# Kernel optimization log

Measured on AMD Instinct MI355X. Metric: run time of the kernel, lower is better.

## Reference

```python
import jax, jax.numpy as jnp
import numpy as np

TEMPERATURE = 0.1


def setup_inputs() -> dict:
    key = jax.random.key(0)
    k1, k2, k3 = jax.random.split(key, 3)
    B, C, D = 8192, 1000, 128
    features = jax.random.normal(k1, (B, D), dtype=jnp.float32)
    features = features / jnp.linalg.norm(features, axis=-1, keepdims=True)
    centers1 = jax.random.normal(k2, (C, D), dtype=jnp.float32)
    centers1 = centers1 / jnp.linalg.norm(centers1, axis=-1, keepdims=True)
    targets = jax.random.randint(k3, (B,), 0, C, dtype=jnp.int64)
    return {"centers1": centers1, "features": features, "targets": targets}


def reference(centers1, features, targets):
    B = features.shape[0]
    C = centers1.shape[0]
    dt = features.dtype

    # concatenated targets: batch targets followed by one target per class center
    t_all = jnp.concatenate([targets, jnp.arange(C, dtype=targets.dtype)])  # [B+C]
    # per-class counts over the concatenated targets (each class >= 1 from its center)
    cls_count = jnp.zeros((C,), dt).at[t_all].add(1.0)

    # positive mask [B, B+C]; zero out self-comparisons on the leading diagonal
    mask = (targets[:, None] == t_all[None, :]).astype(dt)
    logits_mask = jnp.ones((B, B + C), dt).at[jnp.arange(B), jnp.arange(B)].set(0.0)
    mask = mask * logits_mask

    feats_all = jnp.concatenate([features, centers1], axis=0)  # [B+C, D]
    logits = jnp.matmul(features, feats_all.T) / TEMPERATURE    # [B, B+C]
    logits = logits - jax.lax.stop_gradient(jnp.max(logits, axis=1, keepdims=True))

    exp_logits = jnp.exp(logits) * logits_mask
    per_ins_weight = cls_count[t_all][None, :] - mask           # [B, B+C]
    exp_logits_sum = jnp.sum(exp_logits / per_ins_weight, axis=1, keepdims=True)

    log_prob = logits - jnp.log(exp_logits_sum)
    mean_log_prob_pos = jnp.sum(mask * log_prob, axis=1) / jnp.sum(mask, axis=1)
    return -jnp.mean(mean_log_prob_pos)
```

## Files before the change

kernel.cpp:

```cpp
#include <hip/hip_runtime.h>
#include <math.h>

typedef __attribute__((ext_vector_type(8))) short short8;
typedef __attribute__((ext_vector_type(4))) float f32x4;

#define BB 8192
#define CC 1000
#define NN 9192
#define NPAD 9216
#define DD 128
#define RBW 32
#define NSPLIT 8
#define CPB 1152
#define NT 36
#define K2F 14.426950408889634f

#define WS_CLS   0
#define WS_META  1024
#define WS_SPART 37888
#define WS_PPART 103424
#define WS_F2    168960
#define WS_BS    463872

static __device__ __forceinline__ unsigned short f2bf(float x) {
    unsigned int b = __float_as_uint(x);
    unsigned int r = (b + 0x7FFFu + ((b >> 16) & 1u)) >> 16;
    return (unsigned short)r;
}
static __device__ __forceinline__ float fexp2(float x) {
    float r; asm("v_exp_f32 %0, %1" : "=v"(r) : "v"(x)); return r;
}
static __device__ __forceinline__ float flog2(float x) {
    float r; asm("v_log_f32 %0, %1" : "=v"(r) : "v"(x)); return r;
}

__global__ __launch_bounds__(1024) void prep_kernel(
    const float* __restrict__ feats, const float* __restrict__ ctrs,
    const int* __restrict__ tgt, unsigned short* __restrict__ F2,
    int* __restrict__ cls, float4* __restrict__ meta)
{
    const int tid = threadIdx.x;
    if (blockIdx.x < 144) {
        int u = blockIdx.x * 1024 + tid;
        int j = u >> 4, quad = u & 15;
        int k0 = quad * 8;
        float4 v0 = {0.f,0.f,0.f,0.f}, v1 = {0.f,0.f,0.f,0.f};
        if (j < BB) {
            v0 = *(const float4*)&feats[(size_t)j * DD + k0];
            v1 = *(const float4*)&feats[(size_t)j * DD + k0 + 4];
        } else if (j < NN) {
            v0 = *(const float4*)&ctrs[(size_t)(j - BB) * DD + k0];
            v1 = *(const float4*)&ctrs[(size_t)(j - BB) * DD + k0 + 4];
        }
        short8 o;
        o[0]=f2bf(v0.x); o[1]=f2bf(v0.y); o[2]=f2bf(v0.z); o[3]=f2bf(v0.w);
        o[4]=f2bf(v1.x); o[5]=f2bf(v1.y); o[6]=f2bf(v1.z); o[7]=f2bf(v1.w);
        size_t offb = (size_t)((((j >> 4) * 4 + (quad >> 2)) * 64 + (quad & 3) * 16 + (j & 15)) * 8);
        *(short8*)&F2[offb] = o;
        return;
    }

    __shared__ int h[1024];
    h[tid] = 0;
    __syncthreads();
    for (int i = tid; i < BB; i += 1024) atomicAdd(&h[tgt[i]], 1);
    __syncthreads();

    cls[tid] = h[tid];

    for (int j = tid; j < NPAD; j += 1024) {
        float4 m = {__int_as_float(-2), 0.f, 0.f, 0.f};
        if (j < NN) {
            int c = (j < BB) ? tgt[j] : (j - BB);
            int n = h[c] + 1;
            m.x = __int_as_float(c);
            m.y = 1.0f / (float)n;
            m.z = (n > 1) ? 1.0f / (float)(n - 1) : 0.0f;
        }
        meta[j] = m;
    }
}

static __device__ __forceinline__ void loadB32(const unsigned short* __restrict__ F2,
                                               int j0, int lane8, short8 (&buf)[8]) {
#pragma unroll
    for (int fn = 0; fn < 2; ++fn)
#pragma unroll
        for (int ks = 0; ks < 4; ++ks)
            buf[fn * 4 + ks] = *(const short8*)&F2[(size_t)(((((j0 >> 4) + fn) * 4 + ks) * 512) + lane8)];
}

static __device__ __forceinline__ void mfma32(const short8 (&af)[4][2], const short8 (&b)[8],
                                              f32x4 (&acc)[2][2]) {
    const f32x4 z4 = {0.f, 0.f, 0.f, 0.f};
#pragma unroll
    for (int fm = 0; fm < 2; ++fm)
#pragma unroll
        for (int fn = 0; fn < 2; ++fn)
            acc[fm][fn] = __builtin_amdgcn_mfma_f32_16x16x32_bf16(af[0][fm], b[fn * 4], z4, 0, 0, 0);
#pragma unroll
    for (int ks = 1; ks < 4; ++ks)
#pragma unroll
        for (int fm = 0; fm < 2; ++fm)
#pragma unroll
            for (int fn = 0; fn < 2; ++fn)
                acc[fm][fn] = __builtin_amdgcn_mfma_f32_16x16x32_bf16(
                    af[ks][fm], b[fn * 4 + ks], acc[fm][fn], 0, 0, 0);
}

template<bool DIAG>
static __device__ __forceinline__ void epi32(const f32x4 (&acc)[2][2], const float4 (&mt)[2],
                                             int j0, int l15, int rowbase,
                                             const int (&ti)[8],
                                             float (&Sl)[8], float (&Pl)[8]) {
#pragma unroll
    for (int fn = 0; fn < 2; ++fn) {
        const int tj = __float_as_int(mt[fn].x);
        const float r0 = mt[fn].y, r1 = mt[fn].z;
        const int col = j0 + fn * 16 + l15;
#pragma unroll
        for (int fm = 0; fm < 2; ++fm)
#pragma unroll
            for (int q = 0; q < 4; ++q) {
                const int x = fm * 4 + q;
                float d = acc[fm][fn][q];
                float l2 = fmaf(d, K2F, -K2F);
                float e = fexp2(l2);
                bool m = (tj == ti[x]);
                if (DIAG) {
                    bool self = (col == rowbase + fm * 16 + q);
                    if (self) { e = 0.f; m = false; }
                }
                float rw = m ? r1 : r0;
                Sl[x] = fmaf(e, rw, Sl[x]);
                Pl[x] += m ? d : 0.f;
            }
    }
}

__global__ __launch_bounds__(256, 2) void main_kernel(
    const unsigned short* __restrict__ F2, const float4* __restrict__ meta,
    float* __restrict__ S_part, float* __restrict__ P_part)
{
    const int tid  = threadIdx.x;
    const int lane = tid & 63;
    const int wave = tid >> 6;
    const int l15 = lane & 15, l4 = lane >> 4;
    const int lane8 = lane * 8;
    const int row0 = blockIdx.x * (4 * RBW) + wave * RBW;
    const int split = blockIdx.y;
    const int cb = split * CPB;
    const int rowbase = row0 + l4 * 4;

    short8 af[4][2];
#pragma unroll
    for (int fm = 0; fm < 2; ++fm)
#pragma unroll
        for (int ks = 0; ks < 4; ++ks)
            af[ks][fm] = *(const short8*)&F2[(size_t)((((row0 >> 4) + fm) * 4 + ks) * 512 + lane8)];

    int ti[8];
#pragma unroll
    for (int fm = 0; fm < 2; ++fm)
#pragma unroll
        for (int q = 0; q < 4; ++q)
            ti[fm * 4 + q] = __float_as_int(meta[rowbase + fm * 16 + q].x);

    float Sl[8], Pl[8];
#pragma unroll
    for (int x = 0; x < 8; ++x) { Sl[x] = 0.f; Pl[x] = 0.f; }

    short8 bA[8], bB[8];
    float4 mA[2], mB[2];
    loadB32(F2, cb, lane8, bA);
    mA[0] = meta[cb + l15]; mA[1] = meta[cb + 16 + l15];

#pragma unroll 1
    for (int tt = 0; tt < NT; tt += 2) {
        {
            if (tt + 1 < NT) {
                int j = cb + (tt + 1) * 32;
                loadB32(F2, j, lane8, bB);
                mB[0] = meta[j + l15]; mB[1] = meta[j + 16 + l15];
            }
            const int j0 = cb + tt * 32;
            f32x4 acc[2][2];
            mfma32(af, bA, acc);
            if (j0 == row0) epi32<true >(acc, mA, j0, l15, rowbase, ti, Sl, Pl);
            else            epi32<false>(acc, mA, j0, l15, rowbase, ti, Sl, Pl);
        }
        {
            if (tt + 2 < NT) {
                int j = cb + (tt + 2) * 32;
                loadB32(F2, j, lane8, bA);
                mA[0] = meta[j + l15]; mA[1] = meta[j + 16 + l15];
            }
            const int j0 = cb + (tt + 1) * 32;
            f32x4 acc[2][2];
            mfma32(af, bB, acc);
            if (j0 == row0) epi32<true >(acc, mB, j0, l15, rowbase, ti, Sl, Pl);
            else            epi32<false>(acc, mB, j0, l15, rowbase, ti, Sl, Pl);
        }
    }

#pragma unroll
    for (int idx = 0; idx < 8; ++idx) {
        float S = Sl[idx], P = Pl[idx];
#pragma unroll
        for (int off = 1; off < 16; off <<= 1) {
            S += __shfl_xor(S, off, 64);
            P += __shfl_xor(P, off, 64);
        }
        if (l15 == 0) {
            int row = row0 + (idx >> 2) * 16 + l4 * 4 + (idx & 3);
            S_part[(size_t)row * NSPLIT + split] = S;
            P_part[(size_t)row * NSPLIT + split] = P;
        }
    }
}

__global__ __launch_bounds__(256) void final1_kernel(
    const int* __restrict__ tgt, const int* __restrict__ cls,
    const float* __restrict__ S_part, const float* __restrict__ P_part,
    float* __restrict__ bs)
{
    const int tid = threadIdx.x;
    const int i = blockIdx.x * 256 + tid;
    float S = 0.f, P = 0.f;
    const float4* sp = (const float4*)&S_part[(size_t)i * NSPLIT];
    const float4* pp = (const float4*)&P_part[(size_t)i * NSPLIT];
#pragma unroll
    for (int q = 0; q < NSPLIT / 4; ++q) {
        float4 a = sp[q]; S += (a.x + a.y) + (a.z + a.w);
        float4 b = pp[q]; P += (b.x + b.y) + (b.z + b.w);
    }
    const float npos = (float)cls[tgt[i]];
    float lp = fmaf(K2F, P / npos, -K2F) - flog2(S);

#pragma unroll
    for (int off = 1; off < 64; off <<= 1) lp += __shfl_xor(lp, off, 64);
    __shared__ float wsum[4];
    if ((tid & 63) == 0) wsum[tid >> 6] = lp;
    __syncthreads();
    if (tid == 0) bs[blockIdx.x] = wsum[0] + wsum[1] + wsum[2] + wsum[3];
}

__global__ void final2_kernel(const float* __restrict__ bs, float* __restrict__ out) {
    const int t = threadIdx.x;
    float v = (t < 32) ? bs[t] : 0.f;
#pragma unroll
    for (int off = 1; off < 64; off <<= 1) v += __shfl_xor(v, off, 64);
    if (t == 0) out[0] = -0.6931471805599453f * (v / (float)BB);
}

extern "C" void kernel_launch(void* const* d_in, const int* in_sizes, int n_in,
                              void* d_out, int out_size, void* d_ws, size_t ws_size,
                              hipStream_t stream) {
    const float* ctrs  = (const float*)d_in[0];
    const float* feats = (const float*)d_in[1];
    const int*   tgt   = (const int*)d_in[2];
    float* out = (float*)d_out;
    float* ws  = (float*)d_ws;

    int*    cls  = (int*)(ws + WS_CLS);
    float4* meta = (float4*)(ws + WS_META);
    float*  Sp   = ws + WS_SPART;
    float*  Pp   = ws + WS_PPART;
    float*  bs   = ws + WS_BS;
    unsigned short* F2 = (unsigned short*)(ws + WS_F2);

    prep_kernel<<<dim3(145), dim3(1024), 0, stream>>>(feats, ctrs, tgt, F2, cls, meta);
    main_kernel<<<dim3(BB / (4 * RBW), NSPLIT), dim3(256), 0, stream>>>(F2, meta, Sp, Pp);
    final1_kernel<<<dim3(BB / 256), dim3(256), 0, stream>>>(tgt, cls, Sp, Pp, bs);
    final2_kernel<<<dim3(1), dim3(64), 0, stream>>>(bs, out);
}
```

Baseline: 45.43 us.

## Split positive-pair handling into sparse correction kernel, simplify dense epilogue

```diff
diff --git a/kernel.cpp b/kernel.cpp
--- a/kernel.cpp
+++ b/kernel.cpp
@@ -15,12 +15,15 @@
 #define NT 36
 #define K2F 14.426950408889634f
 
-#define WS_CLS   0
-#define WS_META  1024
-#define WS_SPART 37888
-#define WS_PPART 103424
-#define WS_F2    168960
-#define WS_BS    463872
+#define WS_CLS    0
+#define WS_OFF    1024
+#define WS_LIST   2048
+#define WS_RCP0   11264
+#define WS_SCORR  20480
+#define WS_PCORR  28672
+#define WS_SPART  36864
+#define WS_BS     102400
+#define WS_F2     102464
 
 static __device__ __forceinline__ unsigned short f2bf(float x) {
     unsigned int b = __float_as_uint(x);
@@ -37,7 +40,8 @@
 __global__ __launch_bounds__(1024) void prep_kernel(
     const float* __restrict__ feats, const float* __restrict__ ctrs,
     const int* __restrict__ tgt, unsigned short* __restrict__ F2,
-    int* __restrict__ cls, float4* __restrict__ meta)
+    int* __restrict__ cls, int* __restrict__ off, int* __restrict__ list,
+    float* __restrict__ rcp0)
 {
     const int tid = threadIdx.x;
     if (blockIdx.x < 144) {
@@ -61,23 +65,54 @@
     }
 
     __shared__ int h[1024];
+    __shared__ int s[1024];
+    __shared__ int cur[1024];
+    __shared__ int llds[NPAD];
+
     h[tid] = 0;
     __syncthreads();
     for (int i = tid; i < BB; i += 1024) atomicAdd(&h[tgt[i]], 1);
     __syncthreads();
 
-    cls[tid] = h[tid];
+    const int cnt_b = h[tid];
+    cls[tid] = cnt_b;
 
     for (int j = tid; j < NPAD; j += 1024) {
-        float4 m = {__int_as_float(-2), 0.f, 0.f, 0.f};
+        float v = 0.f;
         if (j < NN) {
             int c = (j < BB) ? tgt[j] : (j - BB);
-            int n = h[c] + 1;
-            m.x = __int_as_float(c);
-            m.y = 1.0f / (float)n;
-            m.z = (n > 1) ? 1.0f / (float)(n - 1) : 0.0f;
-        }
-        meta[j] = m;
+            v = 1.0f / (float)(h[c] + 1);
+        }
+        rcp0[j] = v;
+    }
+
+    int v = (tid < CC) ? cnt_b + 1 : 0;
+    s[tid] = v;
+    __syncthreads();
+    for (int d = 1; d < 1024; d <<= 1) {
+        int t = (tid >= d) ? s[tid - d] : 0;
+        __syncthreads();
+        s[tid] += t;
+        __syncthreads();
+    }
+    const int o = s[tid] - v;
+    if (tid < CC) { off[tid] = o; cur[tid] = o; }
+    __syncthreads();
+
+    for (int j = tid; j < NN; j += 1024) {
+        int c = (j < BB) ? tgt[j] : (j - BB);
+        int r = atomicAdd(&cur[c], 1);
+        llds[r] = j;
+    }
+    __syncthreads();
+    for (int p = tid; p < NN; p += 1024) {
+        int e = llds[p];
+        int c = (e < BB) ? tgt[e] : (e - BB);
+        int ob = (c > 0) ? s[c - 1] : 0;
+        int n = h[c] + 1;
+        int rank = 0;
+        for (int m = 0; m < n; ++m) rank += (llds[ob + m] < e);
+        list[ob + rank] = e;
     }
 }
 
@@ -108,39 +143,23 @@
                     af[ks][fm], b[fn * 4 + ks], acc[fm][fn], 0, 0, 0);
 }
 
-template<bool DIAG>
-static __device__ __forceinline__ void epi32(const f32x4 (&acc)[2][2], const float4 (&mt)[2],
-                                             int j0, int l15, int rowbase,
-                                             const int (&ti)[8],
-                                             float (&Sl)[8], float (&Pl)[8]) {
-#pragma unroll
-    for (int fn = 0; fn < 2; ++fn) {
-        const int tj = __float_as_int(mt[fn].x);
-        const float r0 = mt[fn].y, r1 = mt[fn].z;
-        const int col = j0 + fn * 16 + l15;
-#pragma unroll
-        for (int fm = 0; fm < 2; ++fm)
-#pragma unroll
-            for (int q = 0; q < 4; ++q) {
-                const int x = fm * 4 + q;
-                float d = acc[fm][fn][q];
-                float l2 = fmaf(d, K2F, -K2F);
-                float e = fexp2(l2);
-                bool m = (tj == ti[x]);
-                if (DIAG) {
-                    bool self = (col == rowbase + fm * 16 + q);
-                    if (self) { e = 0.f; m = false; }
-                }
-                float rw = m ? r1 : r0;
-                Sl[x] = fmaf(e, rw, Sl[x]);
-                Pl[x] += m ? d : 0.f;
-            }
-    }
+static __device__ __forceinline__ void epi32s(const f32x4 (&acc)[2][2],
+                                              float r0a, float r0b, float (&Sl)[8]) {
+#pragma unroll
+    for (int fm = 0; fm < 2; ++fm)
+#pragma unroll
+        for (int q = 0; q < 4; ++q) {
+            const int x = fm * 4 + q;
+            float l2a = fmaf(acc[fm][0][q], K2F, -K2F);
+            Sl[x] = fmaf(fexp2(l2a), r0a, Sl[x]);
+            float l2b = fmaf(acc[fm][1][q], K2F, -K2F);
+            Sl[x] = fmaf(fexp2(l2b), r0b, Sl[x]);
+        }
 }
 
 __global__ __launch_bounds__(256, 2) void main_kernel(
-    const unsigned short* __restrict__ F2, const float4* __restrict__ meta,
-    float* __restrict__ S_part, float* __restrict__ P_part)
+    const unsigned short* __restrict__ F2, const float* __restrict__ rcp0,
+    float* __restrict__ S_part)
 {
     const int tid  = threadIdx.x;
     const int lane = tid & 63;
@@ -150,7 +169,6 @@
     const int row0 = blockIdx.x * (4 * RBW) + wave * RBW;
     const int split = blockIdx.y;
     const int cb = split * CPB;
-    const int rowbase = row0 + l4 * 4;
 
     short8 af[4][2];
 #pragma unroll
@@ -159,81 +177,95 @@
         for (int ks = 0; ks < 4; ++ks)
             af[ks][fm] = *(const short8*)&F2[(size_t)((((row0 >> 4) + fm) * 4 + ks) * 512 + lane8)];
 
-    int ti[8];
-#pragma unroll
-    for (int fm = 0; fm < 2; ++fm)
-#pragma unroll
-        for (int q = 0; q < 4; ++q)
-            ti[fm * 4 + q] = __float_as_int(meta[rowbase + fm * 16 + q].x);
-
-    float Sl[8], Pl[8];
-#pragma unroll
-    for (int x = 0; x < 8; ++x) { Sl[x] = 0.f; Pl[x] = 0.f; }
+    float Sl[8];
+#pragma unroll
+    for (int x = 0; x < 8; ++x) Sl[x] = 0.f;
 
     short8 bA[8], bB[8];
-    float4 mA[2], mB[2];
+    float r0A0, r0A1, r0B0, r0B1;
     loadB32(F2, cb, lane8, bA);
-    mA[0] = meta[cb + l15]; mA[1] = meta[cb + 16 + l15];
+    r0A0 = rcp0[cb + l15]; r0A1 = rcp0[cb + 16 + l15];
 
 #pragma unroll 1
     for (int tt = 0; tt < NT; tt += 2) {
         {
-            if (tt + 1 < NT) {
-                int j = cb + (tt + 1) * 32;
-                loadB32(F2, j, lane8, bB);
-                mB[0] = meta[j + l15]; mB[1] = meta[j + 16 + l15];
-            }
-            const int j0 = cb + tt * 32;
+            int j = cb + (tt + 1) * 32;
+            loadB32(F2, j, lane8, bB);
+            r0B0 = rcp0[j + l15]; r0B1 = rcp0[j + 16 + l15];
             f32x4 acc[2][2];
             mfma32(af, bA, acc);
-            if (j0 == row0) epi32<true >(acc, mA, j0, l15, rowbase, ti, Sl, Pl);
-            else            epi32<false>(acc, mA, j0, l15, rowbase, ti, Sl, Pl);
+            epi32s(acc, r0A0, r0A1, Sl);
         }
         {
             if (tt + 2 < NT) {
                 int j = cb + (tt + 2) * 32;
                 loadB32(F2, j, lane8, bA);
-                mA[0] = meta[j + l15]; mA[1] = meta[j + 16 + l15];
+                r0A0 = rcp0[j + l15]; r0A1 = rcp0[j + 16 + l15];
             }
-            const int j0 = cb + (tt + 1) * 32;
             f32x4 acc[2][2];
             mfma32(af, bB, acc);
-            if (j0 == row0) epi32<true >(acc, mB, j0, l15, rowbase, ti, Sl, Pl);
-            else            epi32<false>(acc, mB, j0, l15, rowbase, ti, Sl, Pl);
+            epi32s(acc, r0B0, r0B1, Sl);
         }
     }
 
 #pragma unroll
     for (int idx = 0; idx < 8; ++idx) {
-        float S = Sl[idx], P = Pl[idx];
-#pragma unroll
-        for (int off = 1; off < 16; off <<= 1) {
-            S += __shfl_xor(S, off, 64);
-            P += __shfl_xor(P, off, 64);
-        }
+        float S = Sl[idx];
+#pragma unroll
+        for (int off = 1; off < 16; off <<= 1) S += __shfl_xor(S, off, 64);
         if (l15 == 0) {
             int row = row0 + (idx >> 2) * 16 + l4 * 4 + (idx & 3);
             S_part[(size_t)row * NSPLIT + split] = S;
-            P_part[(size_t)row * NSPLIT + split] = P;
-        }
-    }
+        }
+    }
+}
+
+__global__ __launch_bounds__(256) void corr_kernel(
+    const float* __restrict__ feats, const float* __restrict__ ctrs,
+    const int* __restrict__ tgt, const int* __restrict__ cls,
+    const int* __restrict__ off, const int* __restrict__ list,
+    float* __restrict__ Scorr, float* __restrict__ Pcorr)
+{
+    const int wave = threadIdx.x >> 6, lane = threadIdx.x & 63;
+    const int i = blockIdx.x * 4 + wave;
+    const int c = tgt[i];
+    const int n = cls[c];
+    const int o = off[c];
+    const float r0i = 1.0f / (float)(n + 1);
+    const float rd  = 1.0f / (float)n - r0i;
+    const int k0 = lane * 2;
+    const float2 fi = *(const float2*)&feats[(size_t)i * DD + k0];
+
+    float CorrS = 0.f, P = 0.f;
+    for (int idx = 0; idx <= n; ++idx) {
+        int j = list[o + idx];
+        const float* src = (j < BB) ? &feats[(size_t)j * DD + k0]
+                                    : &ctrs[(size_t)(j - BB) * DD + k0];
+        float2 fj = *(const float2*)src;
+        float d = fi.x * fj.x + fi.y * fj.y;
+#pragma unroll
+        for (int s = 1; s < 64; s <<= 1) d += __shfl_xor(d, s, 64);
+        float e = fexp2(fmaf(d, K2F, -K2F));
+        if (j == i) CorrS -= e * r0i;
+        else        { CorrS += e * rd; P += d; }
+    }
+    if (lane == 0) { Scorr[i] = CorrS; Pcorr[i] = P; }
 }
 
 __global__ __launch_bounds__(256) void final1_kernel(
     const int* __restrict__ tgt, const int* __restrict__ cls,
-    const float* __restrict__ S_part, const float* __restrict__ P_part,
-    float* __restrict__ bs)
+    const float* __restrict__ S_part, const float* __restrict__ Scorr,
+    const float* __restrict__ Pcorr, float* __restrict__ bs)
 {
     const int tid = threadIdx.x;
     const int i = blockIdx.x * 256 + tid;
-    float S = 0.f, P = 0.f;
+    float S = Scorr[i];
     const float4* sp = (const float4*)&S_part[(size_t)i * NSPLIT];
-    const float4* pp = (const float4*)&P_part[(size_t)i * NSPLIT];
 #pragma unroll
     for (int q = 0; q < NSPLIT / 4; ++q) {
         float4 a = sp[q]; S += (a.x + a.y) + (a.z + a.w);
-        float4 b = pp[q]; P += (b.x + b.y) + (b.z + b.w);
-    }
+    }
+    const float P = Pcorr[i];
     const float npos = (float)cls[tgt[i]];
     float lp = fmaf(K2F, P / npos, -K2F) - flog2(S);
 
@@ -262,15 +294,19 @@
     float* out = (float*)d_out;
     float* ws  = (float*)d_ws;
 
-    int*    cls  = (int*)(ws + WS_CLS);
-    float4* meta = (float4*)(ws + WS_META);
-    float*  Sp   = ws + WS_SPART;
-    float*  Pp   = ws + WS_PPART;
-    float*  bs   = ws + WS_BS;
+    int*   cls   = (int*)(ws + WS_CLS);
+    int*   off   = (int*)(ws + WS_OFF);
+    int*   list  = (int*)(ws + WS_LIST);
+    float* rcp0  = ws + WS_RCP0;
+    float* Scorr = ws + WS_SCORR;
+    float* Pcorr = ws + WS_PCORR;
+    float* Sp    = ws + WS_SPART;
+    float* bs    = ws + WS_BS;
     unsigned short* F2 = (unsigned short*)(ws + WS_F2);
 
-    prep_kernel<<<dim3(145), dim3(1024), 0, stream>>>(feats, ctrs, tgt, F2, cls, meta);
-    main_kernel<<<dim3(BB / (4 * RBW), NSPLIT), dim3(256), 0, stream>>>(F2, meta, Sp, Pp);
-    final1_kernel<<<dim3(BB / 256), dim3(256), 0, stream>>>(tgt, cls, Sp, Pp, bs);
+    prep_kernel<<<dim3(145), dim3(1024), 0, stream>>>(feats, ctrs, tgt, F2, cls, off, list, rcp0);
+    main_kernel<<<dim3(BB / (4 * RBW), NSPLIT), dim3(256), 0, stream>>>(F2, rcp0, Sp);
+    corr_kernel<<<dim3(BB / 4), dim3(256), 0, stream>>>(feats, ctrs, tgt, cls, off, list, Scorr, Pcorr);
+    final1_kernel<<<dim3(BB / 256), dim3(256), 0, stream>>>(tgt, cls, Sp, Scorr, Pcorr, bs);
     final2_kernel<<<dim3(1), dim3(64), 0, stream>>>(bs, out);
 }
```

Result: slower. 67.62 us (+48.9%).
